# Performance work log

Measured on AMD Instinct MI355X. Metric: run time of the kernel, lower is better.

The kernel has to match this reference:

```python
import jax, jax.numpy as jnp
import numpy as np

IMG_H = IMG_W = 640
NUM_CLASSES = 80
B = 8
NUM_ANCHORS = 76725
MAX_TOTAL = 200          # max_total_size == max_size_per_class
SCORE_TH = 0.5
IOU_TH = 0.5
K_CAND = 256             # per-class candidate pool for NMS (>= max survivors)
VARIANCES = jnp.asarray([0.1, 0.1, 0.2, 0.2], jnp.float32)


def _build_anchors(img_h, img_w):
    # RetinaNet AnchorBox: levels 3..7, 3 ratios x 3 scales, [cx, cy, w, h]
    ratios = [0.5, 1.0, 2.0]
    scales = [2.0 ** x for x in (0.0, 1.0 / 3.0, 2.0 / 3.0)]
    areas = [s * s for s in (32.0, 64.0, 128.0, 256.0, 512.0)]
    out = []
    for lvl, stride in enumerate([2 ** i for i in range(3, 8)]):
        dims = []
        for r in ratios:
            h = np.sqrt(areas[lvl] / r)
            w = areas[lvl] / h
            for s in scales:
                dims.append([w * s, h * s])
        dims = np.asarray(dims, np.float32)                      # [9,2]
        fh = int(np.ceil(img_h / stride)); fw = int(np.ceil(img_w / stride))
        rx = (np.arange(fw, dtype=np.float32) + 0.5) * stride
        ry = (np.arange(fh, dtype=np.float32) + 0.5) * stride
        cx, cy = np.meshgrid(rx, ry)
        centers = np.broadcast_to(np.stack([cx, cy], -1)[:, :, None, :], (fh, fw, 9, 2))
        d = np.broadcast_to(dims[None, None], (fh, fw, 9, 2))
        out.append(np.concatenate([centers, d], -1).reshape(-1, 4))
    return jnp.asarray(np.concatenate(out, 0))                   # [A,4]


def setup_inputs() -> dict:
    key = jax.random.key(0)
    k1, k2 = jax.random.split(key)
    box_pred = jax.random.normal(k1, (B, NUM_ANCHORS, 4), jnp.float32)
    cls_pred = jax.random.normal(k2, (B, NUM_ANCHORS, NUM_CLASSES), jnp.float32)
    anchor_boxes = _build_anchors(IMG_H, IMG_W)
    return {"box_pred": box_pred, "cls_pred": cls_pred, "anchor_boxes": anchor_boxes}


def _iou_one_vs_many(box, boxes):
    # box [4] vs boxes [K,4] in corner format
    lt = jnp.maximum(box[:2], boxes[:, :2])
    rb = jnp.minimum(box[2:], boxes[:, 2:])
    wh = jnp.maximum(rb - lt, 0.0)
    inter = wh[:, 0] * wh[:, 1]
    a1 = (box[2] - box[0]) * (box[3] - box[1])
    a2 = (boxes[:, 2] - boxes[:, 0]) * (boxes[:, 3] - boxes[:, 1])
    return inter / jnp.maximum(a1 + a2 - inter, 1e-8)


def _nms_keep(boxes, scores):
    # boxes [K,4] already sorted by descending score; greedy NMS
    eligible = scores > SCORE_TH
    idx = jnp.arange(K_CAND)

    def body(i, keep):
        iou = _iou_one_vs_many(boxes[i], boxes)
        suppress = (iou > IOU_TH) & (idx > i)
        return jnp.where(keep[i], keep & ~suppress, keep)

    keep = jax.lax.fori_loop(0, K_CAND, body, eligible)
    keep = keep & ((jnp.cumsum(keep) - 1) < MAX_TOTAL)           # max_size_per_class cap
    return keep


def _decode_and_nms(box_pred, cls_pred, anchor_boxes):
    scores_all = jax.nn.sigmoid(cls_pred)                        # [B,A,C]
    # decode: (dx,dy,dw,dh)*variances against [cx,cy,w,h] anchors
    d = box_pred * VARIANCES
    xy = d[..., :2] * anchor_boxes[None, :, 2:] + anchor_boxes[None, :, :2]
    wh = jnp.exp(d[..., 2:]) * anchor_boxes[None, :, 2:]
    boxes = jnp.concatenate([xy - 0.5 * wh, xy + 0.5 * wh], -1)  # [B,A,4] corners

    sc = jnp.swapaxes(scores_all, 1, 2)                          # [B,C,A]
    top_sc, top_idx = jax.lax.top_k(sc, K_CAND)                  # [B,C,K] sorted desc
    cand_boxes = jnp.take_along_axis(boxes[:, None], top_idx[..., None], axis=2)  # [B,C,K,4]

    keep = jax.lax.stop_gradient(jax.vmap(jax.vmap(_nms_keep))(cand_boxes, top_sc))  # [B,C,K]
    sel = jnp.where(keep, top_sc, -1.0)

    flat_sc = sel.reshape(B, -1)                                 # [B,C*K]
    flat_boxes = cand_boxes.reshape(B, -1, 4)
    flat_lbl = jnp.broadcast_to(jnp.arange(NUM_CLASSES)[None, :, None],
                                (B, NUM_CLASSES, K_CAND)).reshape(B, -1)

    fs, fi = jax.lax.top_k(flat_sc, MAX_TOTAL)                   # combine across classes
    out_boxes = jnp.take_along_axis(flat_boxes, fi[..., None], axis=1)
    out_lbl = jnp.take_along_axis(flat_lbl, fi, axis=1).astype(jnp.float32)
    valid = fs > 0.0                                             # pad invalid slots
    return (jnp.where(valid[..., None], out_boxes, 0.0),
            jnp.where(valid, fs, 0.0),
            jnp.where(valid, out_lbl, -1.0))


def reference(box_pred, cls_pred, anchor_boxes):
    return _decode_and_nms(box_pred, cls_pred, anchor_boxes)
```

## Files before the change

### kernel.cpp

```cpp
#include <hip/hip_runtime.h>
#include <math.h>
#include <stdint.h>

typedef unsigned long long u64;
typedef unsigned int u32;

#define NB 8
#define NA 76725
#define NC 80
#define KC 256
#define MAXT 200
#define CAP 2048
#define SORTN 1024
#define TAU 2.0f
#define CHUNK 1024
#define NCHUNK 75
#define BCAP 64
#define CSTRIDE 16

#define OFF_BUFA      0ull
#define OFF_CLASSLIST 10485760ull
#define OFF_C1        11796480ull
#define OFF_CANDBOX   11927552ull
#define OFF_COUNTS    14548992ull

__global__ __launch_bounds__(256) void kfilter(const float* __restrict__ cls,
                                               u64* __restrict__ bufA,
                                               u32* __restrict__ counts) {
  __shared__ u64 bucket[NC][BCAP];
  __shared__ u32 bcnt[NC];
  __shared__ u32 gbase[NC];
  __shared__ u32 pref[NC + 1];

  const int b = blockIdx.x / NCHUNK;
  const int ch = blockIdx.x % NCHUNK;
  const int tid = threadIdx.x;
  const int a0 = ch * CHUNK;
  const int aN = (NA - a0) < CHUNK ? (NA - a0) : CHUNK;

  for (int i = tid; i < NC; i += 256) bcnt[i] = 0;
  __syncthreads();

  const float4* p = (const float4*)(cls + ((size_t)b * NA + a0) * NC);
  const int n4 = aN * (NC / 4);
  for (int i = tid; i < n4; i += 256) {
    float4 v = p[i];
    int a = a0 + i / (NC / 4);
    int c0 = (i % (NC / 4)) * 4;
    float vv[4] = {v.x, v.y, v.z, v.w};
#pragma unroll
    for (int j = 0; j < 4; j++) {
      if (vv[j] > TAU) {
        int c = c0 + j;
        u32 pos = atomicAdd(&bcnt[c], 1u);
        if (pos < BCAP)
          bucket[c][pos] = ((u64)__float_as_uint(vv[j]) << 32) | (u32)a;
      }
    }
  }
  __syncthreads();
  if (tid < NC) {
    u32 n = bcnt[tid];
    if (n > BCAP) n = BCAP;
    bcnt[tid] = n;
    gbase[tid] = atomicAdd(&counts[(b * NC + tid) * CSTRIDE], n);
  }
  __syncthreads();
  if (tid == 0) {
    u32 s = 0;
    for (int c = 0; c < NC; c++) { pref[c] = s; s += bcnt[c]; }
    pref[NC] = s;
  }
  __syncthreads();
  const int total = (int)pref[NC];
  for (int e = tid; e < total; e += 256) {
    int lo = 0, hi = NC;
    while (lo + 1 < hi) { int mid = (lo + hi) >> 1; if ((int)pref[mid] <= e) lo = mid; else hi = mid; }
    int c = lo;
    int loc = e - (int)pref[c];
    u32 gb = gbase[c] + (u32)loc;
    if (gb < CAP)
      bufA[((size_t)(b * NC + c)) * CAP + gb] = bucket[c][loc];
  }
}

__global__ __launch_bounds__(256) void kselect(
    const float* __restrict__ cls, const float* __restrict__ boxp,
    const float* __restrict__ anc, u64* __restrict__ bufA,
    const u32* __restrict__ counts, u64* __restrict__ classList,
    float4* __restrict__ candBox) {
  __shared__ u32 hist[1024];
  __shared__ int sbsum[64];
  __shared__ int sT, sNsel, sExtra;
  __shared__ u64 skey[SORTN];
  __shared__ float4 sBox[KC];
  __shared__ int sElig[KC];

  const int tid = threadIdx.x;
  const int bc = blockIdx.x;
  const int b = bc / NC, c = bc % NC;
  u64* buf = bufA + (size_t)bc * CAP;

  int cnt0 = (int)counts[bc * CSTRIDE];
  if (cnt0 > CAP) cnt0 = CAP;
  int cnt = cnt0;
  if (cnt0 < KC) {
    if (tid == 0) sExtra = 0;
    __syncthreads();
    for (int a = tid; a < NA; a += 256) {
      float x = cls[((size_t)b * NA + a) * NC + c];
      if (x > 0.0f && !(x > TAU)) {
        int pos = cnt0 + atomicAdd(&sExtra, 1);
        if (pos < CAP) buf[pos] = ((u64)__float_as_uint(x) << 32) | (u32)a;
      }
    }
    __syncthreads();
    cnt = cnt0 + sExtra;
  }
  if (cnt > CAP) cnt = CAP;

  for (int i = tid; i < 1024; i += 256) hist[i] = 0;
  if (tid == 0) sNsel = 0;
  __syncthreads();
  for (int e = tid; e < cnt; e += 256) {
    float f = __uint_as_float((u32)(buf[e] >> 32));
    int bin = (int)(f * 170.0f);
    bin = bin < 0 ? 0 : (bin > 1023 ? 1023 : bin);
    atomicAdd(&hist[bin], 1u);
  }
  __syncthreads();
  if (tid < 64) {
    int s = 0;
    for (int i = 0; i < 16; i++) s += (int)hist[tid * 16 + i];
    sbsum[tid] = s;
  }
  __syncthreads();
  if (tid == 0) {
    int acc = 0, sb = 63;
    while (sb >= 0 && acc + sbsum[sb] < KC) { acc += sbsum[sb]; sb--; }
    int T = 0;
    if (sb >= 0) {
      int bin = sb * 16 + 15;
      while (bin > sb * 16 && acc + (int)hist[bin] < KC) {
        acc += (int)hist[bin];
        bin--;
      }
      T = bin;
    }
    sT = T;
  }
  __syncthreads();
  const int T = sT;

  for (int e = tid; e < cnt; e += 256) {
    u64 k = buf[e];
    float f = __uint_as_float((u32)(k >> 32));
    int bin = (int)(f * 170.0f);
    bin = bin < 0 ? 0 : (bin > 1023 ? 1023 : bin);
    if (bin >= T) {
      float sc = 1.0f / (1.0f + expf(-f));
      u32 a = (u32)k;
      int pos = atomicAdd(&sNsel, 1);
      if (pos < SORTN)
        skey[pos] = ((u64)__float_as_uint(sc) << 32) | (0xFFFFFFFFu - a);
    }
  }
  __syncthreads();
  int nsel = sNsel;
  if (nsel > SORTN) nsel = SORTN;
  for (int i = tid; i < SORTN; i += 256)
    if (i >= nsel) skey[i] = 0;
  __syncthreads();

  for (int k = 2; k <= SORTN; k <<= 1) {
    for (int j = k >> 1; j > 0; j >>= 1) {
      for (int t = tid; t < SORTN / 2; t += 256) {
        int i = ((t & ~(j - 1)) << 1) | (t & (j - 1));
        int ixj = i | j;
        u64 x = skey[i], y = skey[ixj];
        bool desc = ((i & k) == 0);
        if (desc ? (x < y) : (x > y)) { skey[i] = y; skey[ixj] = x; }
      }
      __syncthreads();
    }
  }

  {
    u64 k = skey[tid];
    float sc = __uint_as_float((u32)(k >> 32));
    u32 a = 0xFFFFFFFFu - (u32)k;
    int el = (k != 0ull) && (sc > 0.5f);
    if (!el || a >= NA) a = 0;
    float4 p = ((const float4*)boxp)[(size_t)b * NA + a];
    float4 an = ((const float4*)anc)[a];
    float dx = __fmul_rn(p.x, 0.1f), dy = __fmul_rn(p.y, 0.1f);
    float dw = __fmul_rn(p.z, 0.2f), dh = __fmul_rn(p.w, 0.2f);
    float cx = __fadd_rn(__fmul_rn(dx, an.z), an.x);
    float cy = __fadd_rn(__fmul_rn(dy, an.w), an.y);
    float w = __fmul_rn(expf(dw), an.z);
    float h = __fmul_rn(expf(dh), an.w);
    float4 bx;
    bx.x = __fsub_rn(cx, __fmul_rn(0.5f, w));
    bx.y = __fsub_rn(cy, __fmul_rn(0.5f, h));
    bx.z = __fadd_rn(cx, __fmul_rn(0.5f, w));
    bx.w = __fadd_rn(cy, __fmul_rn(0.5f, h));
    sBox[tid] = bx;
    sElig[tid] = el;
    candBox[(size_t)bc * KC + tid] = bx;
  }
  __syncthreads();

  if (tid < 64) {
    const int ln = tid;
    float x1[4], y1[4], x2[4], y2[4], ar[4];
    int keep = 0;
#pragma unroll
    for (int s = 0; s < 4; s++) {
      int j = s * 64 + ln;
      float4 bj = sBox[j];
      x1[s] = bj.x; y1[s] = bj.y; x2[s] = bj.z; y2[s] = bj.w;
      ar[s] = __fmul_rn(__fsub_rn(bj.z, bj.x), __fsub_rn(bj.w, bj.y));
      if (sElig[j]) keep |= (1 << s);
    }
    for (int i = 0; i < KC; i++) {
      int ki = __shfl(keep, i & 63, 64);
      if ((ki >> (i >> 6)) & 1) {
        float4 bi = sBox[i];
        float ai = __fmul_rn(__fsub_rn(bi.z, bi.x), __fsub_rn(bi.w, bi.y));
#pragma unroll
        for (int s = 0; s < 4; s++) {
          int j = s * 64 + ln;
          if (j > i) {
            float lx = fmaxf(bi.x, x1[s]), ly = fmaxf(bi.y, y1[s]);
            float rx = fminf(bi.z, x2[s]), ry = fminf(bi.w, y2[s]);
            float wx = fmaxf(__fsub_rn(rx, lx), 0.0f);
            float wy = fmaxf(__fsub_rn(ry, ly), 0.0f);
            float inter = __fmul_rn(wx, wy);
            float uni = fmaxf(__fsub_rn(__fadd_rn(ai, ar[s]), inter), 1e-8f);
            float iou = __fdiv_rn(inter, uni);
            if (iou > 0.5f) keep &= ~(1 << s);
          }
        }
      }
    }
    u64 m[4];
#pragma unroll
    for (int s = 0; s < 4; s++) m[s] = __ballot((keep >> s) & 1);
    int tot = 0;
#pragma unroll
    for (int s = 0; s < 4; s++) tot += __popcll(m[s]);
    int keptTotal = tot < MAXT ? tot : MAXT;
    u64 lmask = (1ull << ln) - 1ull;
    int base = 0;
#pragma unroll
    for (int s = 0; s < 4; s++) {
      int j = s * 64 + ln;
      int cum = base + (int)__popcll(m[s] & lmask);
      if (((keep >> s) & 1) && cum < MAXT) {
        u64 hi = skey[j] >> 32;
        classList[(size_t)bc * KC + cum] =
            (hi << 32) | (u64)(0xFFFFFFFFu - (u32)(c * KC + j));
      }
      base += (int)__popcll(m[s]);
    }
    for (int t2 = ln; t2 < KC; t2 += 64)
      if (t2 >= keptTotal) classList[(size_t)bc * KC + t2] = 0;
  }
}

__device__ __forceinline__ void merge_step(u64* acc, const u64* cur, int t) {
  u64 x = acc[t], y = cur[KC - 1 - t];
  acc[t] = x > y ? x : y;
  __syncthreads();
  for (int s = 128; s >= 1; s >>= 1) {
    if (t < 128) {
      int i = ((t & ~(s - 1)) << 1) | (t & (s - 1));
      u64 a = acc[i], b = acc[i + s];
      if (a < b) { acc[i] = b; acc[i + s] = a; }
    }
    __syncthreads();
  }
}

__global__ __launch_bounds__(256) void kmerge1(const u64* __restrict__ classList,
                                               u64* __restrict__ c1) {
  __shared__ u64 acc[KC], cur[KC];
  int t = threadIdx.x;
  int b = blockIdx.x >> 3, g = blockIdx.x & 7;
  const u64* base = classList + (size_t)(b * NC + g * 10) * KC;
  acc[t] = base[t];
  __syncthreads();
  for (int m = 1; m < 10; m++) {
    cur[t] = base[(size_t)m * KC + t];
    __syncthreads();
    merge_step(acc, cur, t);
  }
  c1[(size_t)blockIdx.x * KC + t] = acc[t];
}

__global__ __launch_bounds__(256) void kmerge2(const u64* __restrict__ c1,
                                               const float4* __restrict__ candBox,
                                               float* __restrict__ out) {
  __shared__ u64 acc[KC], cur[KC];
  int t = threadIdx.x, b = blockIdx.x;
  const u64* base = c1 + (size_t)b * 8 * KC;
  acc[t] = base[t];
  __syncthreads();
  for (int m = 1; m < 8; m++) {
    cur[t] = base[(size_t)m * KC + t];
    __syncthreads();
    merge_step(acc, cur, t);
  }
  if (t < MAXT) {
    u64 k = acc[t];
    float4 bx = make_float4(0.f, 0.f, 0.f, 0.f);
    float sc = 0.0f, lb = -1.0f;
    if (k != 0ull) {
      sc = __uint_as_float((u32)(k >> 32));
      u32 flat = 0xFFFFFFFFu - (u32)k;
      int cc = (int)(flat >> 8), kk = (int)(flat & 255u);
      bx = candBox[((size_t)b * NC + cc) * KC + kk];
      lb = (float)cc;
    }
    float* ob = out + ((size_t)b * MAXT + t) * 4;
    ob[0] = bx.x; ob[1] = bx.y; ob[2] = bx.z; ob[3] = bx.w;
    out[NB * MAXT * 4 + b * MAXT + t] = sc;
    out[NB * MAXT * 4 + NB * MAXT + b * MAXT + t] = lb;
  }
}

extern "C" void kernel_launch(void* const* d_in, const int* in_sizes, int n_in,
                              void* d_out, int out_size, void* d_ws,
                              size_t ws_size, hipStream_t stream) {
  const float* boxp = (const float*)d_in[0];
  const float* cls = (const float*)d_in[1];
  const float* anc = (const float*)d_in[2];
  char* ws = (char*)d_ws;
  u64* bufA = (u64*)(ws + OFF_BUFA);
  u64* classList = (u64*)(ws + OFF_CLASSLIST);
  u64* c1 = (u64*)(ws + OFF_C1);
  float4* candBox = (float4*)(ws + OFF_CANDBOX);
  u32* counts = (u32*)(ws + OFF_COUNTS);

  hipMemsetAsync(counts, 0, NB * NC * CSTRIDE * sizeof(u32), stream);
  kfilter<<<NB * NCHUNK, 256, 0, stream>>>(cls, bufA, counts);
  kselect<<<NB * NC, 256, 0, stream>>>(cls, boxp, anc, bufA, counts, classList,
                                       candBox);
  kmerge1<<<NB * 8, 256, 0, stream>>>(classList, c1);
  kmerge2<<<NB, 256, 0, stream>>>(c1, candBox, (float*)d_out);
}
```

Measured before the change: 434.0 us.

## Fuse merge kernels into wave-shuffle merge, shrink sort, stage buffer in LDS

Several changes land at once. The two cross-class merge kernels become a single kernel that merges in registers with wave shuffles. kfilter uses smaller chunks and loads four float4 values per thread before processing them. kselect copies the candidate buffer into LDS, sorts 512 keys with one compare per thread, precomputes box areas, and makes the NMS inner loop branch-free by computing IoU unconditionally. Cutting SORTN to 512 and BCAP to 48 may change results when candidates overflow, and the eligibility check sc>0.5 is now implied by k!=0 since scores come from logits above zero.

```diff
diff --git a/kernel.cpp b/kernel.cpp
--- a/kernel.cpp
+++ b/kernel.cpp
@@ -11,18 +11,33 @@
 #define KC 256
 #define MAXT 200
 #define CAP 2048
-#define SORTN 1024
+#define SORTN 512
 #define TAU 2.0f
-#define CHUNK 1024
-#define NCHUNK 75
-#define BCAP 64
+#define CHUNK 512
+#define NCHUNK 150
+#define BCAP 48
 #define CSTRIDE 16
 
 #define OFF_BUFA      0ull
 #define OFF_CLASSLIST 10485760ull
-#define OFF_C1        11796480ull
-#define OFF_CANDBOX   11927552ull
-#define OFF_COUNTS    14548992ull
+#define OFF_CANDBOX   11796480ull
+#define OFF_COUNTS    14417920ull
+
+__device__ __forceinline__ void kf_proc(float4 v, int i, int a0,
+                                        u64 (*bucket)[BCAP], u32* bcnt) {
+  int a = a0 + i / (NC / 4);
+  int c0 = (i % (NC / 4)) * 4;
+  float vv[4] = {v.x, v.y, v.z, v.w};
+#pragma unroll
+  for (int j = 0; j < 4; j++) {
+    if (vv[j] > TAU) {
+      int c = c0 + j;
+      u32 pos = atomicAdd(&bcnt[c], 1u);
+      if (pos < BCAP)
+        bucket[c][pos] = ((u64)__float_as_uint(vv[j]) << 32) | (u32)a;
+    }
+  }
+}
 
 __global__ __launch_bounds__(256) void kfilter(const float* __restrict__ cls,
                                                u64* __restrict__ bufA,
@@ -43,20 +58,17 @@
 
   const float4* p = (const float4*)(cls + ((size_t)b * NA + a0) * NC);
   const int n4 = aN * (NC / 4);
-  for (int i = tid; i < n4; i += 256) {
-    float4 v = p[i];
-    int a = a0 + i / (NC / 4);
-    int c0 = (i % (NC / 4)) * 4;
-    float vv[4] = {v.x, v.y, v.z, v.w};
-#pragma unroll
-    for (int j = 0; j < 4; j++) {
-      if (vv[j] > TAU) {
-        int c = c0 + j;
-        u32 pos = atomicAdd(&bcnt[c], 1u);
-        if (pos < BCAP)
-          bucket[c][pos] = ((u64)__float_as_uint(vv[j]) << 32) | (u32)a;
-      }
-    }
+  for (int i0 = tid; i0 < n4; i0 += 1024) {
+    float4 v0, v1, v2, v3;
+    const bool g1 = i0 + 256 < n4, g2 = i0 + 512 < n4, g3 = i0 + 768 < n4;
+    v0 = p[i0];
+    if (g1) v1 = p[i0 + 256];
+    if (g2) v2 = p[i0 + 512];
+    if (g3) v3 = p[i0 + 768];
+    kf_proc(v0, i0, a0, bucket, bcnt);
+    if (g1) kf_proc(v1, i0 + 256, a0, bucket, bcnt);
+    if (g2) kf_proc(v2, i0 + 512, a0, bucket, bcnt);
+    if (g3) kf_proc(v3, i0 + 768, a0, bucket, bcnt);
   }
   __syncthreads();
   if (tid < NC) {
@@ -89,12 +101,13 @@
     const float* __restrict__ anc, u64* __restrict__ bufA,
     const u32* __restrict__ counts, u64* __restrict__ classList,
     float4* __restrict__ candBox) {
+  __shared__ u64 sbuf[CAP];
   __shared__ u32 hist[1024];
   __shared__ int sbsum[64];
   __shared__ int sT, sNsel, sExtra;
   __shared__ u64 skey[SORTN];
   __shared__ float4 sBox[KC];
-  __shared__ int sElig[KC];
+  __shared__ float sAr[KC];
 
   const int tid = threadIdx.x;
   const int bc = blockIdx.x;
@@ -121,9 +134,11 @@
 
   for (int i = tid; i < 1024; i += 256) hist[i] = 0;
   if (tid == 0) sNsel = 0;
-  __syncthreads();
+  for (int e = tid; e < cnt; e += 256) sbuf[e] = buf[e];
+  __syncthreads();
+
   for (int e = tid; e < cnt; e += 256) {
-    float f = __uint_as_float((u32)(buf[e] >> 32));
+    float f = __uint_as_float((u32)(sbuf[e] >> 32));
     int bin = (int)(f * 170.0f);
     bin = bin < 0 ? 0 : (bin > 1023 ? 1023 : bin);
     atomicAdd(&hist[bin], 1u);
@@ -153,7 +168,7 @@
   const int T = sT;
 
   for (int e = tid; e < cnt; e += 256) {
-    u64 k = buf[e];
+    u64 k = sbuf[e];
     float f = __uint_as_float((u32)(k >> 32));
     int bin = (int)(f * 170.0f);
     bin = bin < 0 ? 0 : (bin > 1023 ? 1023 : bin);
@@ -174,23 +189,19 @@
 
   for (int k = 2; k <= SORTN; k <<= 1) {
     for (int j = k >> 1; j > 0; j >>= 1) {
-      for (int t = tid; t < SORTN / 2; t += 256) {
-        int i = ((t & ~(j - 1)) << 1) | (t & (j - 1));
-        int ixj = i | j;
-        u64 x = skey[i], y = skey[ixj];
-        bool desc = ((i & k) == 0);
-        if (desc ? (x < y) : (x > y)) { skey[i] = y; skey[ixj] = x; }
-      }
+      int i = ((tid & ~(j - 1)) << 1) | (tid & (j - 1));
+      int ixj = i | j;
+      u64 x = skey[i], y = skey[ixj];
+      bool desc = ((i & k) == 0);
+      if (desc ? (x < y) : (x > y)) { skey[i] = y; skey[ixj] = x; }
       __syncthreads();
     }
   }
 
   {
     u64 k = skey[tid];
-    float sc = __uint_as_float((u32)(k >> 32));
     u32 a = 0xFFFFFFFFu - (u32)k;
-    int el = (k != 0ull) && (sc > 0.5f);
-    if (!el || a >= NA) a = 0;
+    if (k == 0ull || a >= NA) a = 0;
     float4 p = ((const float4*)boxp)[(size_t)b * NA + a];
     float4 an = ((const float4*)anc)[a];
     float dx = __fmul_rn(p.x, 0.1f), dy = __fmul_rn(p.y, 0.1f);
@@ -205,7 +216,7 @@
     bx.z = __fadd_rn(cx, __fmul_rn(0.5f, w));
     bx.w = __fadd_rn(cy, __fmul_rn(0.5f, h));
     sBox[tid] = bx;
-    sElig[tid] = el;
+    sAr[tid] = __fmul_rn(__fsub_rn(bx.z, bx.x), __fsub_rn(bx.w, bx.y));
     candBox[(size_t)bc * KC + tid] = bx;
   }
   __syncthreads();
@@ -219,29 +230,27 @@
       int j = s * 64 + ln;
       float4 bj = sBox[j];
       x1[s] = bj.x; y1[s] = bj.y; x2[s] = bj.z; y2[s] = bj.w;
-      ar[s] = __fmul_rn(__fsub_rn(bj.z, bj.x), __fsub_rn(bj.w, bj.y));
-      if (sElig[j]) keep |= (1 << s);
+      ar[s] = sAr[j];
+      if (skey[j] != 0ull) keep |= (1 << s);
     }
     for (int i = 0; i < KC; i++) {
+      float4 bi = sBox[i];
+      float ai = sAr[i];
+      int sup = 0;
+#pragma unroll
+      for (int s = 0; s < 4; s++) {
+        int j = s * 64 + ln;
+        float lx = fmaxf(bi.x, x1[s]), ly = fmaxf(bi.y, y1[s]);
+        float rx = fminf(bi.z, x2[s]), ry = fminf(bi.w, y2[s]);
+        float wx = fmaxf(__fsub_rn(rx, lx), 0.0f);
+        float wy = fmaxf(__fsub_rn(ry, ly), 0.0f);
+        float inter = __fmul_rn(wx, wy);
+        float uni = fmaxf(__fsub_rn(__fadd_rn(ai, ar[s]), inter), 1e-8f);
+        float iou = __fdiv_rn(inter, uni);
+        if (j > i && iou > 0.5f) sup |= (1 << s);
+      }
       int ki = __shfl(keep, i & 63, 64);
-      if ((ki >> (i >> 6)) & 1) {
-        float4 bi = sBox[i];
-        float ai = __fmul_rn(__fsub_rn(bi.z, bi.x), __fsub_rn(bi.w, bi.y));
-#pragma unroll
-        for (int s = 0; s < 4; s++) {
-          int j = s * 64 + ln;
-          if (j > i) {
-            float lx = fmaxf(bi.x, x1[s]), ly = fmaxf(bi.y, y1[s]);
-            float rx = fminf(bi.z, x2[s]), ry = fminf(bi.w, y2[s]);
-            float wx = fmaxf(__fsub_rn(rx, lx), 0.0f);
-            float wy = fmaxf(__fsub_rn(ry, ly), 0.0f);
-            float inter = __fmul_rn(wx, wy);
-            float uni = fmaxf(__fsub_rn(__fadd_rn(ai, ar[s]), inter), 1e-8f);
-            float iou = __fdiv_rn(inter, uni);
-            if (iou > 0.5f) keep &= ~(1 << s);
-          }
-        }
-      }
+      if ((ki >> (i >> 6)) & 1) keep &= ~sup;
     }
     u64 m[4];
 #pragma unroll
@@ -268,51 +277,73 @@
   }
 }
 
-__device__ __forceinline__ void merge_step(u64* acc, const u64* cur, int t) {
-  u64 x = acc[t], y = cur[KC - 1 - t];
-  acc[t] = x > y ? x : y;
-  __syncthreads();
-  for (int s = 128; s >= 1; s >>= 1) {
-    if (t < 128) {
-      int i = ((t & ~(s - 1)) << 1) | (t & (s - 1));
-      u64 a = acc[i], b = acc[i + s];
-      if (a < b) { acc[i] = b; acc[i + s] = a; }
-    }
-    __syncthreads();
-  }
-}
-
-__global__ __launch_bounds__(256) void kmerge1(const u64* __restrict__ classList,
-                                               u64* __restrict__ c1) {
-  __shared__ u64 acc[KC], cur[KC];
-  int t = threadIdx.x;
-  int b = blockIdx.x >> 3, g = blockIdx.x & 7;
-  const u64* base = classList + (size_t)(b * NC + g * 10) * KC;
-  acc[t] = base[t];
-  __syncthreads();
-  for (int m = 1; m < 10; m++) {
-    cur[t] = base[(size_t)m * KC + t];
-    __syncthreads();
-    merge_step(acc, cur, t);
-  }
-  c1[(size_t)blockIdx.x * KC + t] = acc[t];
-}
-
-__global__ __launch_bounds__(256) void kmerge2(const u64* __restrict__ c1,
-                                               const float4* __restrict__ candBox,
-                                               float* __restrict__ out) {
-  __shared__ u64 acc[KC], cur[KC];
-  int t = threadIdx.x, b = blockIdx.x;
-  const u64* base = c1 + (size_t)b * 8 * KC;
-  acc[t] = base[t];
-  __syncthreads();
-  for (int m = 1; m < 8; m++) {
-    cur[t] = base[(size_t)m * KC + t];
-    __syncthreads();
-    merge_step(acc, cur, t);
-  }
-  if (t < MAXT) {
-    u64 k = acc[t];
+__device__ __forceinline__ u64 shfl64(u64 v, int src) {
+  int lo = __shfl((int)(u32)v, src, 64);
+  int hi = __shfl((int)(v >> 32), src, 64);
+  return ((u64)(u32)hi << 32) | (u32)lo;
+}
+__device__ __forceinline__ u64 shflxor64(u64 v, int mask) {
+  int lo = __shfl_xor((int)(u32)v, mask, 64);
+  int hi = __shfl_xor((int)(v >> 32), mask, 64);
+  return ((u64)(u32)hi << 32) | (u32)lo;
+}
+#define CSWAP(a, b) { if ((a) < (b)) { u64 _t = (a); (a) = (b); (b) = _t; } }
+
+__device__ __forceinline__ void wave_merge(u64 acc[4], const u64 cur[4], int ln) {
+  u64 t0 = shfl64(cur[3], 63 - ln);
+  u64 t1 = shfl64(cur[2], 63 - ln);
+  u64 t2 = shfl64(cur[1], 63 - ln);
+  u64 t3 = shfl64(cur[0], 63 - ln);
+  acc[0] = acc[0] > t0 ? acc[0] : t0;
+  acc[1] = acc[1] > t1 ? acc[1] : t1;
+  acc[2] = acc[2] > t2 ? acc[2] : t2;
+  acc[3] = acc[3] > t3 ? acc[3] : t3;
+  CSWAP(acc[0], acc[2]); CSWAP(acc[1], acc[3]);
+  CSWAP(acc[0], acc[1]); CSWAP(acc[2], acc[3]);
+#pragma unroll
+  for (int s = 32; s >= 1; s >>= 1) {
+#pragma unroll
+    for (int k = 0; k < 4; k++) {
+      u64 o = shflxor64(acc[k], s);
+      u64 mx = acc[k] > o ? acc[k] : o;
+      u64 mn = acc[k] < o ? acc[k] : o;
+      acc[k] = ((ln & s) == 0) ? mx : mn;
+    }
+  }
+}
+
+__global__ __launch_bounds__(256) void kmerge(const u64* __restrict__ classList,
+                                              const float4* __restrict__ candBox,
+                                              float* __restrict__ out) {
+  __shared__ u64 lds[4 * KC];
+  const int tid = threadIdx.x, b = blockIdx.x;
+  const int w = tid >> 6, ln = tid & 63;
+  const u64* base = classList + ((size_t)b * NC + w * 20) * KC;
+  u64 acc[4];
+#pragma unroll
+  for (int k = 0; k < 4; k++) acc[k] = base[k * 64 + ln];
+  for (int m = 1; m < 20; m++) {
+    u64 cur[4];
+#pragma unroll
+    for (int k = 0; k < 4; k++) cur[k] = base[(size_t)m * KC + k * 64 + ln];
+    wave_merge(acc, cur, ln);
+  }
+#pragma unroll
+  for (int k = 0; k < 4; k++) lds[w * KC + k * 64 + ln] = acc[k];
+  __syncthreads();
+  if (w == 0) {
+    for (int m = 1; m < 4; m++) {
+      u64 cur[4];
+#pragma unroll
+      for (int k = 0; k < 4; k++) cur[k] = lds[m * KC + k * 64 + ln];
+      wave_merge(acc, cur, ln);
+    }
+#pragma unroll
+    for (int k = 0; k < 4; k++) lds[k * 64 + ln] = acc[k];
+  }
+  __syncthreads();
+  if (tid < MAXT) {
+    u64 k = lds[tid];
     float4 bx = make_float4(0.f, 0.f, 0.f, 0.f);
     float sc = 0.0f, lb = -1.0f;
     if (k != 0ull) {
@@ -322,10 +353,10 @@
       bx = candBox[((size_t)b * NC + cc) * KC + kk];
       lb = (float)cc;
     }
-    float* ob = out + ((size_t)b * MAXT + t) * 4;
+    float* ob = out + ((size_t)b * MAXT + tid) * 4;
     ob[0] = bx.x; ob[1] = bx.y; ob[2] = bx.z; ob[3] = bx.w;
-    out[NB * MAXT * 4 + b * MAXT + t] = sc;
-    out[NB * MAXT * 4 + NB * MAXT + b * MAXT + t] = lb;
+    out[NB * MAXT * 4 + b * MAXT + tid] = sc;
+    out[NB * MAXT * 4 + NB * MAXT + b * MAXT + tid] = lb;
   }
 }
 
@@ -338,7 +369,6 @@
   char* ws = (char*)d_ws;
   u64* bufA = (u64*)(ws + OFF_BUFA);
   u64* classList = (u64*)(ws + OFF_CLASSLIST);
-  u64* c1 = (u64*)(ws + OFF_C1);
   float4* candBox = (float4*)(ws + OFF_CANDBOX);
   u32* counts = (u32*)(ws + OFF_COUNTS);
 
@@ -346,6 +376,5 @@
   kfilter<<<NB * NCHUNK, 256, 0, stream>>>(cls, bufA, counts);
   kselect<<<NB * NC, 256, 0, stream>>>(cls, boxp, anc, bufA, counts, classList,
                                        candBox);
-  kmerge1<<<NB * 8, 256, 0, stream>>>(classList, c1);
-  kmerge2<<<NB, 256, 0, stream>>>(c1, candBox, (float*)d_out);
-}
+  kmerge<<<NB, 256, 0, stream>>>(classList, candBox, (float*)d_out);
+}
```

After: 410.5 us. 5.4% less time.
